# Kernel tuning notes

Measured on AMD Instinct MI355X. Metric: run time of the kernel, lower is better.

## Reference

```python
import jax, jax.numpy as jnp
import numpy as np


def _make_area_table():
    # Surrogate for create_table_neighbour_code_to_surface_area((1,1,1)):
    # a fixed 256-entry lookup that is exactly 0 for the all-empty (0) and
    # all-full (255) neighbour codes and strictly positive otherwise, which
    # preserves the structure the loss relies on (gt_surface = area > 0,
    # gt_foreground = code==255, gt_background = code==0).
    pop = np.array([bin(c).count("1") for c in range(256)], dtype=np.float32)
    return (0.5 * np.minimum(pop, 8.0 - pop)).astype(np.float32)


def _conv3d(x, w):
    # x: [B,1,D,H,W], w: [1,1,2,2,2], VALID 2x2x2 sliding window
    return jax.lax.conv_general_dilated(
        x, w, window_strides=(1, 1, 1), padding="VALID",
        dimension_numbers=("NCDHW", "OIDHW", "NCDHW"))


def setup_inputs() -> dict:
    key = jax.random.key(0)
    k1, k2 = jax.random.split(key)
    B, D, H, W = 2, 128, 256, 256
    preds = jax.random.normal(k1, (B, 1, D, H, W), dtype=jnp.float32)
    targets = jax.random.randint(k2, (B, 1, D, H, W), 0, 2).astype(jnp.float32)
    power = (2.0 ** jnp.arange(8, dtype=jnp.float32)).reshape(1, 1, 2, 2, 2)
    kernel = jnp.ones((1, 1, 2, 2, 2), dtype=jnp.float32)
    area = jnp.asarray(_make_area_table())
    return {"preds": preds, "targets": targets, "power": power,
            "kernel": kernel, "area": area}


def reference(preds, targets, power, kernel, area):
    eps = 1e-5
    bsz = preds.shape[0]

    # log-prob that all 8 voxels of each 2x2x2 cube are foreground / background
    fg = jnp.exp(_conv3d(jax.nn.log_sigmoid(preds), kernel)).reshape(bsz, -1)
    bg = jnp.exp(_conv3d(jax.nn.log_sigmoid(-preds), kernel)).reshape(bsz, -1)
    surf = 1.0 - fg - bg

    # neighbour codes from binary targets (no grad path)
    codes = jax.lax.stop_gradient(_conv3d(targets, power)).astype(jnp.int32).reshape(bsz, -1)
    gt_area = area[codes.reshape(-1)].reshape(bsz, -1)
    gt_fg = (codes == 255).astype(jnp.float32)
    gt_bg = (codes == 0).astype(jnp.float32)
    gt_surf = (gt_area > 0).astype(jnp.float32)

    fg_dice = (2.0 * jnp.sum(fg * gt_fg, -1) + eps) / (jnp.sum(fg, -1) + jnp.sum(gt_fg, -1) + eps)
    bg_dice = (2.0 * jnp.sum(bg * gt_bg, -1) + eps) / (jnp.sum(bg, -1) + jnp.sum(gt_bg, -1) + eps)
    surf_dice = (2.0 * jnp.sum(surf * gt_area, -1) + eps) / (jnp.sum((surf + gt_surf) * gt_area, -1) + eps)

    dice = (fg_dice + bg_dice + surf_dice) / 3.0
    return 1.0 - jnp.mean(dice)
```

## Files before the change

kernel.cpp:

```cpp
#include <hip/hip_runtime.h>

typedef float f2 __attribute__((ext_vector_type(2)));

#define DD 128
#define HH 256
#define WW 256
#define OD 127
#define SLICE_F (HH*WW)
#define CHUNK 8
#define TEN_B 3072
#define BUF_B 6144
#define WAVE_B 12288
#define AS1 __attribute__((address_space(1)))
#define AS3 __attribute__((address_space(3)))

#define VMCNT0() asm volatile("s_waitcnt vmcnt(0)" ::: "memory")
#define VMCNT6() asm volatile("s_waitcnt vmcnt(6)" ::: "memory")

struct Sl { f2 uu2[4]; f2 vv2[4]; f2 ps[4]; };

__device__ __forceinline__ void stage_slice(const float* __restrict__ pB,
                                            const float* __restrict__ tB,
                                            int s, char* lb, int h0w, int lane)
{
    const size_t so = ((size_t)s << 16) + (size_t)(lane << 2);
    #pragma unroll
    for (int r = 0; r < 3; ++r) {
        const int grow = min(h0w + r, HH - 1);
        const float* gp = pB + so + ((size_t)grow << 8);
        const float* gt = tB + so + ((size_t)grow << 8);
        __builtin_amdgcn_global_load_lds((const AS1 void*)gp,
            (AS3 void*)(lb + r * 1024 + lane * 16), 16, 0, 0);
        __builtin_amdgcn_global_load_lds((const AS1 void*)gt,
            (AS3 void*)(lb + TEN_B + r * 1024 + lane * 16), 16, 0, 0);
    }
}

__device__ __forceinline__ void make_sl(const char* lb, int lane, Sl& S)
{
    const float* sp = (const float*)lb;
    const float* st = (const float*)(lb + TEN_B);
    const int co = lane << 2;
    const float4 p0 = *(const float4*)(sp + co);
    const float4 p1 = *(const float4*)(sp + co + 256);
    const float4 p2 = *(const float4*)(sp + co + 512);
    const float4 t0 = *(const float4*)(st + co);
    const float4 t1 = *(const float4*)(st + co + 256);
    const float4 t2 = *(const float4*)(st + co + 512);

    float u0x=__expf(p0.x), u0y=__expf(p0.y), u0z=__expf(p0.z), u0w=__expf(p0.w);
    float u1x=__expf(p1.x), u1y=__expf(p1.y), u1z=__expf(p1.z), u1w=__expf(p1.w);
    float u2x=__expf(p2.x), u2y=__expf(p2.y), u2z=__expf(p2.z), u2w=__expf(p2.w);

    f2 uA0 = {u0x,u1x}, uB0 = {u1x,u2x};
    f2 uA1 = {u0y,u1y}, uB1 = {u1y,u2y};
    f2 uA2 = {u0z,u1z}, uB2 = {u1z,u2z};
    f2 uA3 = {u0w,u1w}, uB3 = {u1w,u2w};

    f2 W0 = uA0*uB0, W1 = uA1*uB1, W2 = uA2*uB2, W3 = uA3*uB3;
    f2 Q0 = (uA0+1.f)*(uB0+1.f);
    f2 Q1 = (uA1+1.f)*(uB1+1.f);
    f2 Q2 = (uA2+1.f)*(uB2+1.f);
    f2 Q3 = (uA3+1.f)*(uB3+1.f);
    f2 W4, Q4;
    W4.x = __shfl_down(W0.x, 1); W4.y = __shfl_down(W0.y, 1);
    Q4.x = __shfl_down(Q0.x, 1); Q4.y = __shfl_down(Q0.y, 1);

    S.uu2[0]=W0*W1; S.uu2[1]=W1*W2; S.uu2[2]=W2*W3; S.uu2[3]=W3*W4;
    S.vv2[0]=Q0*Q1; S.vv2[1]=Q1*Q2; S.vv2[2]=Q2*Q3; S.vv2[3]=Q3*Q4;

    f2 cs0 = {t0.x+t1.x, t1.x+t2.x};
    f2 cs1 = {t0.y+t1.y, t1.y+t2.y};
    f2 cs2 = {t0.z+t1.z, t1.z+t2.z};
    f2 cs3 = {t0.w+t1.w, t1.w+t2.w};
    f2 cs4; cs4.x = __shfl_down(cs0.x, 1); cs4.y = __shfl_down(cs0.y, 1);
    S.ps[0]=cs0+cs1; S.ps[1]=cs1+cs2; S.ps[2]=cs2+cs3; S.ps[3]=cs3+cs4;
}

__device__ __forceinline__ void do_cubes(const Sl& P, const Sl& C,
        const f2 vAll, const f2 v3,
        f2& aFG, f2& aF255, f2& aBG, f2& aBG0, f2& aSFA,
        f2& c255, f2& c0, f2& cMN)
{
    #pragma unroll
    for (int j = 0; j < 4; ++j) {
        f2 E = P.uu2[j] * C.uu2[j];
        f2 Q = P.vv2[j] * C.vv2[j];
        f2 vj = (j == 3) ? v3 : vAll;
        f2 r; r.x = __builtin_amdgcn_rcpf(Q.x); r.y = __builtin_amdgcn_rcpf(Q.y);
        r *= vj;
        f2 fg = E * r;
        f2 pop = P.ps[j] + C.ps[j];
        f2 i255, i0, mn;
        i255.x = fmaxf(pop.x - 7.f, 0.f); i255.y = fmaxf(pop.y - 7.f, 0.f);
        i0.x   = fmaxf(1.f - pop.x, 0.f); i0.y   = fmaxf(1.f - pop.y, 0.f);
        mn.x   = 4.f - fabsf(pop.x - 4.f); mn.y = 4.f - fabsf(pop.y - 4.f);
        mn *= vj;
        aFG  += fg;
        aBG  += r;
        aF255 = fg * i255 + aF255;
        aBG0  = r  * i0   + aBG0;
        c255  = i255 * vj + c255;
        c0    = i0   * vj + c0;
        aSFA  = (fg + r) * mn + aSFA;
        cMN  += mn;
    }
}

#define LAYER(SRC, DST)                                                        \
    do {                                                                       \
        if (t + 2 <= NT) {                                                     \
            stage_slice(pB, tB, d0 + t + 2, wb + (t & 1) * BUF_B, h0w, lane);  \
            VMCNT6();               \
        } else {                                                               \
            VMCNT0();                                                          \
        }                                                                      \
        __builtin_amdgcn_sched_barrier(0);                                     \
        make_sl(wb + ((t + 1) & 1) * BUF_B, lane, DST);                        \
        do_cubes(SRC, DST, vAll, v3, aFG, aF255, aBG, aBG0, aSFA, c255, c0, cMN); \
    } while (0)

__global__ __launch_bounds__(256, 3)
void loss_main(const float* __restrict__ preds,
               const float* __restrict__ targets,
               float* __restrict__ ws)
{
    __shared__ __align__(16) char smem[4 * WAVE_B];
    __shared__ float red[32];

    const int lane = threadIdx.x & 63;
    const int wv   = threadIdx.x >> 6;
    char* wb = smem + wv * WAVE_B;

    const int nid = ((blockIdx.x & 7) << 7) + (blockIdx.x >> 3);
    const int x = nid & 31;
    const int y = (nid >> 5) & 15;
    const int b = nid >> 9;

    const int h0w = (x << 3) + (wv << 1);
    const int d0  = y << 3;
    const int NT  = min(CHUNK, OD - d0);

    const float* pB = preds   + (size_t)b * DD * SLICE_F;
    const float* tB = targets + (size_t)b * DD * SLICE_F;

    const float rv1 = (h0w + 1 < HH - 1) ? 1.f : 0.f;
    const float v63 = (lane == 63) ? 0.f : 1.f;
    const f2 vAll = {1.f, rv1};
    const f2 v3   = {v63, v63 * rv1};

    f2 aFG={0,0}, aF255={0,0}, aBG={0,0}, aBG0={0,0}, aSFA={0,0};
    f2 c255={0,0}, c0={0,0}, cMN={0,0};

    stage_slice(pB, tB, d0,     wb,         h0w, lane);
    stage_slice(pB, tB, d0 + 1, wb + BUF_B, h0w, lane);
    VMCNT6();
    __builtin_amdgcn_sched_barrier(0);

    Sl A, B;
    make_sl(wb, lane, A);

    int t = 0;
    for (;;) {
        LAYER(A, B);
        if (++t >= NT) break;
        LAYER(B, A);
        if (++t >= NT) break;
    }

    float acc[8] = {aFG.x+aFG.y, aF255.x+aF255.y, c255.x+c255.y,
                    aBG.x+aBG.y, aBG0.x+aBG0.y,   c0.x+c0.y,
                    aSFA.x+aSFA.y, cMN.x+cMN.y};
    #pragma unroll
    for (int i = 0; i < 8; ++i) {
        float v = acc[i];
        #pragma unroll
        for (int off = 32; off > 0; off >>= 1) v += __shfl_xor(v, off);
        acc[i] = v;
    }
    float mine = acc[0];
    mine = (lane == 1) ? acc[1] : mine;
    mine = (lane == 2) ? acc[2] : mine;
    mine = (lane == 3) ? acc[3] : mine;
    mine = (lane == 4) ? acc[4] : mine;
    mine = (lane == 5) ? acc[5] : mine;
    mine = (lane == 6) ? acc[6] : mine;
    mine = (lane == 7) ? acc[7] : mine;
    if (lane < 8) red[wv * 8 + lane] = mine;
    __syncthreads();
    if (wv == 0 && lane < 8)
        ws[nid * 8 + lane] = red[lane] + red[8 + lane] + red[16 + lane] + red[24 + lane];
}

__global__ void loss_final(const float* __restrict__ ws, float* __restrict__ out)
{
    __shared__ float part[16][17];
    __shared__ float S[16];
    const int tid = threadIdx.x;
    const int c = tid >> 4, sub = tid & 15;
    const int bb = c >> 3, s = c & 7;
    float v = 0.f;
    #pragma unroll 4
    for (int k = 0; k < 32; ++k) {
        int nid = bb * 512 + sub * 32 + k;
        v += ws[nid * 8 + s];
    }
    part[c][sub] = v;
    __syncthreads();
    if (tid < 16) {
        float q = 0.f;
        #pragma unroll
        for (int i = 0; i < 16; ++i) q += part[tid][i];
        S[tid] = q;
    }
    __syncthreads();
    if (tid == 0) {
        const float eps = 1e-5f;
        float dice = 0.f;
        #pragma unroll
        for (int b2 = 0; b2 < 2; ++b2) {
            const float* q = S + b2 * 8;
            float fg_dice = (2.f*q[1] + eps) / (q[0] + q[2] + eps);
            float bg_dice = (2.f*q[4] + eps) / (q[3] + q[5] + eps);
            float q6 = 0.5f * q[6];
            float q7 = 0.5f * q[7];
            float ss = q7 - q6;
            float sf_dice = (2.f*ss + eps) / (ss + q7 + eps);
            dice += fg_dice + bg_dice + sf_dice;
        }
        out[0] = 1.f - dice * (1.f/6.f);
    }
}

extern "C" void kernel_launch(void* const* d_in, const int* in_sizes, int n_in,
                              void* d_out, int out_size, void* d_ws, size_t ws_size,
                              hipStream_t stream)
{
    const float* preds   = (const float*)d_in[0];
    const float* targets = (const float*)d_in[1];
    float* ws = (float*)d_ws;

    loss_main<<<1024, 256, 0, stream>>>(preds, targets, ws);
    loss_final<<<1, 256, 0, stream>>>(ws, (float*)d_out);
}
```

Baseline: 35.40 us.

## Process four output rows per wave to cut halo row reloads

Each wave now stages five input rows per slice and computes four output rows instead of three rows for two outputs. Neighbouring waves therefore reload fewer shared halo rows, and the exp work per output drops. The grid is halved to 512 blocks with launch bounds lowered to two blocks per CU, which doubles LDS per wave and raises register pressure. The per-block shared-memory reduction and syncthreads are removed: each wave writes its own partials to the workspace, and the final kernel sums more entries.

```diff
diff --git a/kernel.cpp b/kernel.cpp
--- a/kernel.cpp
+++ b/kernel.cpp
@@ -1,6 +1,6 @@
 #include <hip/hip_runtime.h>
 
-typedef float f2 __attribute__((ext_vector_type(2)));
+typedef float f4v __attribute__((ext_vector_type(4)));
 
 #define DD 128
 #define HH 256
@@ -8,16 +8,17 @@
 #define OD 127
 #define SLICE_F (HH*WW)
 #define CHUNK 8
-#define TEN_B 3072
-#define BUF_B 6144
-#define WAVE_B 12288
+#define TEN_B 5120
+#define BUF_B 10240
+#define WAVE_B 20480
 #define AS1 __attribute__((address_space(1)))
 #define AS3 __attribute__((address_space(3)))
 
-#define VMCNT0() asm volatile("s_waitcnt vmcnt(0)" ::: "memory")
-#define VMCNT6() asm volatile("s_waitcnt vmcnt(6)" ::: "memory")
-
-struct Sl { f2 uu2[4]; f2 vv2[4]; f2 ps[4]; };
+#define WAITS() asm volatile("s_waitcnt vmcnt(10)" ::: "memory")
+#define WAIT0() asm volatile("s_waitcnt vmcnt(0)"  ::: "memory")
+#define SB0()   __builtin_amdgcn_sched_barrier(0)
+
+struct Sl { f4v uu2[4]; f4v vv2[4]; f4v ps[4]; };
 
 __device__ __forceinline__ void stage_slice(const float* __restrict__ pB,
                                             const float* __restrict__ tB,
@@ -25,7 +26,7 @@
 {
     const size_t so = ((size_t)s << 16) + (size_t)(lane << 2);
     #pragma unroll
-    for (int r = 0; r < 3; ++r) {
+    for (int r = 0; r < 5; ++r) {
         const int grow = min(h0w + r, HH - 1);
         const float* gp = pB + so + ((size_t)grow << 8);
         const float* gt = tB + so + ((size_t)grow << 8);
@@ -44,57 +45,70 @@
     const float4 p0 = *(const float4*)(sp + co);
     const float4 p1 = *(const float4*)(sp + co + 256);
     const float4 p2 = *(const float4*)(sp + co + 512);
+    const float4 p3 = *(const float4*)(sp + co + 768);
+    const float4 p4 = *(const float4*)(sp + co + 1024);
     const float4 t0 = *(const float4*)(st + co);
     const float4 t1 = *(const float4*)(st + co + 256);
     const float4 t2 = *(const float4*)(st + co + 512);
-
-    float u0x=__expf(p0.x), u0y=__expf(p0.y), u0z=__expf(p0.z), u0w=__expf(p0.w);
-    float u1x=__expf(p1.x), u1y=__expf(p1.y), u1z=__expf(p1.z), u1w=__expf(p1.w);
-    float u2x=__expf(p2.x), u2y=__expf(p2.y), u2z=__expf(p2.z), u2w=__expf(p2.w);
-
-    f2 uA0 = {u0x,u1x}, uB0 = {u1x,u2x};
-    f2 uA1 = {u0y,u1y}, uB1 = {u1y,u2y};
-    f2 uA2 = {u0z,u1z}, uB2 = {u1z,u2z};
-    f2 uA3 = {u0w,u1w}, uB3 = {u1w,u2w};
-
-    f2 W0 = uA0*uB0, W1 = uA1*uB1, W2 = uA2*uB2, W3 = uA3*uB3;
-    f2 Q0 = (uA0+1.f)*(uB0+1.f);
-    f2 Q1 = (uA1+1.f)*(uB1+1.f);
-    f2 Q2 = (uA2+1.f)*(uB2+1.f);
-    f2 Q3 = (uA3+1.f)*(uB3+1.f);
-    f2 W4, Q4;
-    W4.x = __shfl_down(W0.x, 1); W4.y = __shfl_down(W0.y, 1);
-    Q4.x = __shfl_down(Q0.x, 1); Q4.y = __shfl_down(Q0.y, 1);
-
-    S.uu2[0]=W0*W1; S.uu2[1]=W1*W2; S.uu2[2]=W2*W3; S.uu2[3]=W3*W4;
-    S.vv2[0]=Q0*Q1; S.vv2[1]=Q1*Q2; S.vv2[2]=Q2*Q3; S.vv2[3]=Q3*Q4;
-
-    f2 cs0 = {t0.x+t1.x, t1.x+t2.x};
-    f2 cs1 = {t0.y+t1.y, t1.y+t2.y};
-    f2 cs2 = {t0.z+t1.z, t1.z+t2.z};
-    f2 cs3 = {t0.w+t1.w, t1.w+t2.w};
-    f2 cs4; cs4.x = __shfl_down(cs0.x, 1); cs4.y = __shfl_down(cs0.y, 1);
-    S.ps[0]=cs0+cs1; S.ps[1]=cs1+cs2; S.ps[2]=cs2+cs3; S.ps[3]=cs3+cs4;
+    const float4 t3 = *(const float4*)(st + co + 768);
+    const float4 t4 = *(const float4*)(st + co + 1024);
+
+    float e0x=__expf(p0.x), e1x=__expf(p1.x), e2x=__expf(p2.x), e3x=__expf(p3.x), e4x=__expf(p4.x);
+    float e0y=__expf(p0.y), e1y=__expf(p1.y), e2y=__expf(p2.y), e3y=__expf(p3.y), e4y=__expf(p4.y);
+    float e0z=__expf(p0.z), e1z=__expf(p1.z), e2z=__expf(p2.z), e3z=__expf(p3.z), e4z=__expf(p4.z);
+    float e0w=__expf(p0.w), e1w=__expf(p1.w), e2w=__expf(p2.w), e3w=__expf(p3.w), e4w=__expf(p4.w);
+
+    f4v Wx = {e0x*e1x, e1x*e2x, e2x*e3x, e3x*e4x};
+    f4v Wy = {e0y*e1y, e1y*e2y, e2y*e3y, e3y*e4y};
+    f4v Wz = {e0z*e1z, e1z*e2z, e2z*e3z, e3z*e4z};
+    f4v Ww = {e0w*e1w, e1w*e2w, e2w*e3w, e3w*e4w};
+    f4v Qx = {(1.f+e0x)*(1.f+e1x), (1.f+e1x)*(1.f+e2x), (1.f+e2x)*(1.f+e3x), (1.f+e3x)*(1.f+e4x)};
+    f4v Qy = {(1.f+e0y)*(1.f+e1y), (1.f+e1y)*(1.f+e2y), (1.f+e2y)*(1.f+e3y), (1.f+e3y)*(1.f+e4y)};
+    f4v Qz = {(1.f+e0z)*(1.f+e1z), (1.f+e1z)*(1.f+e2z), (1.f+e2z)*(1.f+e3z), (1.f+e3z)*(1.f+e4z)};
+    f4v Qw = {(1.f+e0w)*(1.f+e1w), (1.f+e1w)*(1.f+e2w), (1.f+e2w)*(1.f+e3w), (1.f+e3w)*(1.f+e4w)};
+
+    f4v W4, Q4;
+    W4.x = __shfl_down(Wx.x, 1); W4.y = __shfl_down(Wx.y, 1);
+    W4.z = __shfl_down(Wx.z, 1); W4.w = __shfl_down(Wx.w, 1);
+    Q4.x = __shfl_down(Qx.x, 1); Q4.y = __shfl_down(Qx.y, 1);
+    Q4.z = __shfl_down(Qx.z, 1); Q4.w = __shfl_down(Qx.w, 1);
+
+    S.uu2[0]=Wx*Wy; S.uu2[1]=Wy*Wz; S.uu2[2]=Wz*Ww; S.uu2[3]=Ww*W4;
+    S.vv2[0]=Qx*Qy; S.vv2[1]=Qy*Qz; S.vv2[2]=Qz*Qw; S.vv2[3]=Qw*Q4;
+
+    f4v cx = {t0.x+t1.x, t1.x+t2.x, t2.x+t3.x, t3.x+t4.x};
+    f4v cy = {t0.y+t1.y, t1.y+t2.y, t2.y+t3.y, t3.y+t4.y};
+    f4v cz = {t0.z+t1.z, t1.z+t2.z, t2.z+t3.z, t3.z+t4.z};
+    f4v cw = {t0.w+t1.w, t1.w+t2.w, t2.w+t3.w, t3.w+t4.w};
+    f4v c4;
+    c4.x = __shfl_down(cx.x, 1); c4.y = __shfl_down(cx.y, 1);
+    c4.z = __shfl_down(cx.z, 1); c4.w = __shfl_down(cx.w, 1);
+    S.ps[0]=cx+cy; S.ps[1]=cy+cz; S.ps[2]=cz+cw; S.ps[3]=cw+c4;
 }
 
 __device__ __forceinline__ void do_cubes(const Sl& P, const Sl& C,
-        const f2 vAll, const f2 v3,
-        f2& aFG, f2& aF255, f2& aBG, f2& aBG0, f2& aSFA,
-        f2& c255, f2& c0, f2& cMN)
+        const f4v vAll, const f4v v3,
+        f4v& aFG, f4v& aF255, f4v& aBG, f4v& aBG0, f4v& aSFA,
+        f4v& c255, f4v& c0, f4v& cMN)
 {
     #pragma unroll
     for (int j = 0; j < 4; ++j) {
-        f2 E = P.uu2[j] * C.uu2[j];
-        f2 Q = P.vv2[j] * C.vv2[j];
-        f2 vj = (j == 3) ? v3 : vAll;
-        f2 r; r.x = __builtin_amdgcn_rcpf(Q.x); r.y = __builtin_amdgcn_rcpf(Q.y);
+        f4v E = P.uu2[j] * C.uu2[j];
+        f4v Q = P.vv2[j] * C.vv2[j];
+        f4v vj = (j == 3) ? v3 : vAll;
+        f4v r;
+        r.x = __builtin_amdgcn_rcpf(Q.x); r.y = __builtin_amdgcn_rcpf(Q.y);
+        r.z = __builtin_amdgcn_rcpf(Q.z); r.w = __builtin_amdgcn_rcpf(Q.w);
         r *= vj;
-        f2 fg = E * r;
-        f2 pop = P.ps[j] + C.ps[j];
-        f2 i255, i0, mn;
+        f4v fg = E * r;
+        f4v pop = P.ps[j] + C.ps[j];
+        f4v i255, i0, mn;
         i255.x = fmaxf(pop.x - 7.f, 0.f); i255.y = fmaxf(pop.y - 7.f, 0.f);
+        i255.z = fmaxf(pop.z - 7.f, 0.f); i255.w = fmaxf(pop.w - 7.f, 0.f);
         i0.x   = fmaxf(1.f - pop.x, 0.f); i0.y   = fmaxf(1.f - pop.y, 0.f);
+        i0.z   = fmaxf(1.f - pop.z, 0.f); i0.w   = fmaxf(1.f - pop.w, 0.f);
         mn.x   = 4.f - fabsf(pop.x - 4.f); mn.y = 4.f - fabsf(pop.y - 4.f);
+        mn.z   = 4.f - fabsf(pop.z - 4.f); mn.w = 4.f - fabsf(pop.w - 4.f);
         mn *= vj;
         aFG  += fg;
         aBG  += r;
@@ -111,51 +125,53 @@
     do {                                                                       \
         if (t + 2 <= NT) {                                                     \
             stage_slice(pB, tB, d0 + t + 2, wb + (t & 1) * BUF_B, h0w, lane);  \
-            VMCNT6();               \
+            WAITS();               \
         } else {                                                               \
-            VMCNT0();                                                          \
+            WAIT0();                                                           \
         }                                                                      \
-        __builtin_amdgcn_sched_barrier(0);                                     \
+        SB0();                                                                 \
         make_sl(wb + ((t + 1) & 1) * BUF_B, lane, DST);                        \
         do_cubes(SRC, DST, vAll, v3, aFG, aF255, aBG, aBG0, aSFA, c255, c0, cMN); \
     } while (0)
 
-__global__ __launch_bounds__(256, 3)
+__global__ __launch_bounds__(256, 2)
 void loss_main(const float* __restrict__ preds,
                const float* __restrict__ targets,
                float* __restrict__ ws)
 {
     __shared__ __align__(16) char smem[4 * WAVE_B];
-    __shared__ float red[32];
 
     const int lane = threadIdx.x & 63;
     const int wv   = threadIdx.x >> 6;
     char* wb = smem + wv * WAVE_B;
 
-    const int nid = ((blockIdx.x & 7) << 7) + (blockIdx.x >> 3);
-    const int x = nid & 31;
-    const int y = (nid >> 5) & 15;
-    const int b = nid >> 9;
-
-    const int h0w = (x << 3) + (wv << 1);
+    const int nid = ((blockIdx.x & 7) << 6) + (blockIdx.x >> 3);
+    const int x = nid & 15;
+    const int y = (nid >> 4) & 15;
+    const int b = nid >> 8;
+
+    const int h0w = (x << 4) + (wv << 2);
     const int d0  = y << 3;
     const int NT  = min(CHUNK, OD - d0);
 
     const float* pB = preds   + (size_t)b * DD * SLICE_F;
     const float* tB = targets + (size_t)b * DD * SLICE_F;
 
-    const float rv1 = (h0w + 1 < HH - 1) ? 1.f : 0.f;
     const float v63 = (lane == 63) ? 0.f : 1.f;
-    const f2 vAll = {1.f, rv1};
-    const f2 v3   = {v63, v63 * rv1};
-
-    f2 aFG={0,0}, aF255={0,0}, aBG={0,0}, aBG0={0,0}, aSFA={0,0};
-    f2 c255={0,0}, c0={0,0}, cMN={0,0};
+    f4v vAll;
+    vAll.x = (h0w     < HH - 1) ? 1.f : 0.f;
+    vAll.y = (h0w + 1 < HH - 1) ? 1.f : 0.f;
+    vAll.z = (h0w + 2 < HH - 1) ? 1.f : 0.f;
+    vAll.w = (h0w + 3 < HH - 1) ? 1.f : 0.f;
+    const f4v v3 = vAll * v63;
+
+    f4v aFG={0,0,0,0}, aF255=aFG, aBG=aFG, aBG0=aFG, aSFA=aFG;
+    f4v c255=aFG, c0=aFG, cMN=aFG;
 
     stage_slice(pB, tB, d0,     wb,         h0w, lane);
     stage_slice(pB, tB, d0 + 1, wb + BUF_B, h0w, lane);
-    VMCNT6();
-    __builtin_amdgcn_sched_barrier(0);
+    WAITS();
+    SB0();
 
     Sl A, B;
     make_sl(wb, lane, A);
@@ -168,9 +184,15 @@
         if (++t >= NT) break;
     }
 
-    float acc[8] = {aFG.x+aFG.y, aF255.x+aF255.y, c255.x+c255.y,
-                    aBG.x+aBG.y, aBG0.x+aBG0.y,   c0.x+c0.y,
-                    aSFA.x+aSFA.y, cMN.x+cMN.y};
+    float acc[8];
+    acc[0] = (aFG.x  + aFG.y)  + (aFG.z  + aFG.w);
+    acc[1] = (aF255.x+ aF255.y)+ (aF255.z+ aF255.w);
+    acc[2] = (c255.x + c255.y) + (c255.z + c255.w);
+    acc[3] = (aBG.x  + aBG.y)  + (aBG.z  + aBG.w);
+    acc[4] = (aBG0.x + aBG0.y) + (aBG0.z + aBG0.w);
+    acc[5] = (c0.x   + c0.y)   + (c0.z   + c0.w);
+    acc[6] = (aSFA.x + aSFA.y) + (aSFA.z + aSFA.w);
+    acc[7] = (cMN.x  + cMN.y)  + (cMN.z  + cMN.w);
     #pragma unroll
     for (int i = 0; i < 8; ++i) {
         float v = acc[i];
@@ -186,31 +208,30 @@
     mine = (lane == 5) ? acc[5] : mine;
     mine = (lane == 6) ? acc[6] : mine;
     mine = (lane == 7) ? acc[7] : mine;
-    if (lane < 8) red[wv * 8 + lane] = mine;
-    __syncthreads();
-    if (wv == 0 && lane < 8)
-        ws[nid * 8 + lane] = red[lane] + red[8 + lane] + red[16 + lane] + red[24 + lane];
+    if (lane < 8)
+        ws[(nid * 4 + wv) * 8 + lane] = mine;
 }
 
 __global__ void loss_final(const float* __restrict__ ws, float* __restrict__ out)
 {
-    __shared__ float part[16][17];
+    __shared__ float fin[256];
     __shared__ float S[16];
     const int tid = threadIdx.x;
-    const int c = tid >> 4, sub = tid & 15;
-    const int bb = c >> 3, s = c & 7;
+    const int s = tid & 7, k = tid >> 3;
+    const int b2 = k >> 4;
     float v = 0.f;
     #pragma unroll 4
-    for (int k = 0; k < 32; ++k) {
-        int nid = bb * 512 + sub * 32 + k;
-        v += ws[nid * 8 + s];
-    }
-    part[c][sub] = v;
+    for (int j = 0; j < 64; ++j) {
+        int g = b2 * 1024 + (k & 15) * 64 + j;
+        v += ws[g * 8 + s];
+    }
+    fin[tid] = v;
     __syncthreads();
     if (tid < 16) {
+        const int bb = tid >> 3, s2 = tid & 7;
         float q = 0.f;
         #pragma unroll
-        for (int i = 0; i < 16; ++i) q += part[tid][i];
+        for (int k2 = 0; k2 < 16; ++k2) q += fin[(((bb << 4) + k2) << 3) | s2];
         S[tid] = q;
     }
     __syncthreads();
@@ -218,8 +239,8 @@
         const float eps = 1e-5f;
         float dice = 0.f;
         #pragma unroll
-        for (int b2 = 0; b2 < 2; ++b2) {
-            const float* q = S + b2 * 8;
+        for (int bb = 0; bb < 2; ++bb) {
+            const float* q = S + bb * 8;
             float fg_dice = (2.f*q[1] + eps) / (q[0] + q[2] + eps);
             float bg_dice = (2.f*q[4] + eps) / (q[3] + q[5] + eps);
             float q6 = 0.5f * q[6];
@@ -240,6 +261,6 @@
     const float* targets = (const float*)d_in[1];
     float* ws = (float*)d_ws;
 
-    loss_main<<<1024, 256, 0, stream>>>(preds, targets, ws);
+    loss_main<<<512, 256, 0, stream>>>(preds, targets, ws);
     loss_final<<<1, 256, 0, stream>>>(ws, (float*)d_out);
 }
```

Result: slower. 37.41 us (+5.7%).
